# Optimization experiments

Measured on AMD Instinct MI355X. Metric: run time of the kernel, lower is better.

Reference implementation:

```python
import jax, jax.numpy as jnp
import numpy as np

BATCH = 4096
NUM_CLASSES = 10000
FEAT_DIM = 512


def setup_inputs() -> dict:
    key = jax.random.key(0)
    k1, k2, k3 = jax.random.split(key, 3)
    x = jax.random.normal(k1, (BATCH, FEAT_DIM), dtype=jnp.float32)
    labels = jax.random.randint(k2, (BATCH,), 0, NUM_CLASSES)
    centers = jax.random.normal(k3, (NUM_CLASSES, FEAT_DIM), dtype=jnp.float32)
    lr = jnp.array([0.1], dtype=jnp.float32)
    return {"x": x, "labels": labels, "centers": centers, "lr": lr}


def reference(x, labels, centers, lr):
    batch, feat_dim = x.shape
    n_classes = centers.shape[0]

    # --- center update (vectorized replacement of the per-class/per-sample double loop) ---
    # A_j = count_j * centers[j] - sum_{i: label_i==j} x_i ;  delta_j = A_j / (1 + count_j)
    ones = jnp.ones((batch,), dtype=x.dtype)
    counts = jax.ops.segment_sum(ones, labels, num_segments=n_classes)          # [C]
    sum_x = jax.ops.segment_sum(x, labels, num_segments=n_classes)              # [C, D]
    delta = (counts[:, None] * centers - sum_x) / (1.0 + counts[:, None])       # [C, D]
    # torch wraps the result in a fresh nn.Parameter -> detached from autograd graph
    centers_new = jax.lax.stop_gradient(centers - lr[0] * delta)

    # --- pairwise squared distances, then 1/(1+d) ---
    d = (jnp.sum(x * x, axis=1, keepdims=True)                                   # [B, 1]
         + jnp.sum(centers_new * centers_new, axis=1)[None, :]                   # [1, C]
         - 2.0 * (x @ centers_new.T))                                            # [B, C]
    d = 1.0 / (1.0 + d)

    # --- masked reduction: row sum minus the own-class entry, clamped ---
    row_sum = d.sum(axis=1)                                                      # [B]
    own = jnp.take_along_axis(d, labels[:, None], axis=1)[:, 0]                  # [B]
    dist = jnp.clip(row_sum - own, 1e-12, 1e12)
    return dist.mean()
```

## Files before the change

### kernel.cpp

```cpp
#include <hip/hip_runtime.h>
#include <hip/hip_bf16.h>

#define BATCH 4096
#define NCLS  10000
#define CPAD  10240
#define FDIM  512
#define MAXL  32

typedef float f32x4 __attribute__((ext_vector_type(4)));
typedef int   ix4   __attribute__((ext_vector_type(4)));
typedef int   ix8   __attribute__((ext_vector_type(8)));

__device__ static inline void gld_lds16(const void* g, void* l) {
    __builtin_amdgcn_global_load_lds(
        (const __attribute__((address_space(1))) void*)g,
        (__attribute__((address_space(3))) void*)l, 16, 0, 0);
}

__device__ static inline unsigned int fp4e(float v) {
    unsigned int s = (__float_as_uint(v) >> 31) << 3;
    float a = fabsf(v);
    unsigned int c;
    if      (a < 1.25f) c = (a < 0.75f) ? (a < 0.25f ? 0u : 1u) : 2u;
    else if (a < 2.5f)  c = (a < 1.75f) ? 3u : 4u;
    else                c = (a < 3.5f) ? 5u : (a < 5.f ? 6u : 7u);
    return s | c;
}

__device__ static inline int pdst4(int row, int k) {
    return (row >> 4) * 4096 + (k >> 7) * 1024
         + ((k >> 5) & 3) * 256 + (row & 15) * 16 + ((k & 31) >> 1);
}

__global__ void build_lists(const int* __restrict__ labels, int* __restrict__ cnt,
                            int* __restrict__ lists) {
    int i = blockIdx.x * 256 + threadIdx.x;
    int lab = labels[i];
    int p = atomicAdd(&cnt[lab], 1);
    if (p < MAXL) lists[lab * MAXL + p] = i;
}

__global__ void prep_all(const float* __restrict__ x, const int* __restrict__ cnt,
                         const int* __restrict__ lists,
                         const float* __restrict__ centers, const float* __restrict__ lr,
                         unsigned char* __restrict__ xq, float* __restrict__ xnorm,
                         unsigned char* __restrict__ cq, float* __restrict__ cnorm,
                         float* __restrict__ out) {
    const int wid = threadIdx.x >> 6, lane = threadIdx.x & 63;
    const int idx = blockIdx.x * 4 + wid;
    if (blockIdx.x == 0 && threadIdx.x == 0) out[0] = 0.f;

    if (idx < BATCH) {
        int i = idx;
        const float4* xr4 = (const float4*)&x[(size_t)i * FDIM + lane * 8];
        float4 a = xr4[0], b = xr4[1];
        unsigned int d = fp4e(a.x) | (fp4e(a.y) << 4) | (fp4e(a.z) << 8)  | (fp4e(a.w) << 12)
                       | (fp4e(b.x) << 16) | (fp4e(b.y) << 20) | (fp4e(b.z) << 24) | (fp4e(b.w) << 28);
        *(unsigned int*)(xq + pdst4(i, lane * 8)) = d;
        float s = a.x*a.x + a.y*a.y + a.z*a.z + a.w*a.w + b.x*b.x + b.y*b.y + b.z*b.z + b.w*b.w;
#pragma unroll
        for (int m = 1; m < 64; m <<= 1) s += __shfl_xor(s, m);
        if (lane == 0) xnorm[i] = s;
        return;
    }
    int j = idx - BATCH;
    if (j >= NCLS) {
        *(unsigned int*)(cq + pdst4(j, lane * 8)) = 0;
        if (lane == 0) cnorm[j] = 1e30f;
        return;
    }
    __shared__ int idxs[4][MAXL];
    int cfull = cnt[j];
    int c = cfull > MAXL ? MAXL : cfull;
    if (lane < c) idxs[wid][lane] = lists[j * MAXL + lane];
    if (lane == 0 && c > 1) {
        for (int a2 = 1; a2 < c; ++a2) {
            int v = idxs[wid][a2]; int b2 = a2 - 1;
            while (b2 >= 0 && idxs[wid][b2] > v) { idxs[wid][b2 + 1] = idxs[wid][b2]; --b2; }
            idxs[wid][b2 + 1] = v;
        }
    }
    float cf  = (float)cfull;
    float lr0 = lr[0];
    float inv = 1.f / (1.f + cf);
    const float4* cr4 = (const float4*)&centers[(size_t)j * FDIM + lane * 8];
    float4 ca = cr4[0], cb = cr4[1];
    float4 sa = {0.f, 0.f, 0.f, 0.f}, sb = {0.f, 0.f, 0.f, 0.f};
    for (int q = 0; q < c; ++q) {
        const float4* xr4 = (const float4*)&x[(size_t)idxs[wid][q] * FDIM + lane * 8];
        float4 xa = xr4[0], xb = xr4[1];
        sa.x += xa.x; sa.y += xa.y; sa.z += xa.z; sa.w += xa.w;
        sb.x += xb.x; sb.y += xb.y; sb.z += xb.z; sb.w += xb.w;
    }
    float n[8];
    n[0] = ca.x - lr0 * (cf * ca.x - sa.x) * inv;
    n[1] = ca.y - lr0 * (cf * ca.y - sa.y) * inv;
    n[2] = ca.z - lr0 * (cf * ca.z - sa.z) * inv;
    n[3] = ca.w - lr0 * (cf * ca.w - sa.w) * inv;
    n[4] = cb.x - lr0 * (cf * cb.x - sb.x) * inv;
    n[5] = cb.y - lr0 * (cf * cb.y - sb.y) * inv;
    n[6] = cb.z - lr0 * (cf * cb.z - sb.z) * inv;
    n[7] = cb.w - lr0 * (cf * cb.w - sb.w) * inv;
    unsigned int d = 0;
    float cn2 = 0.f;
#pragma unroll
    for (int q = 0; q < 8; ++q) { d |= fp4e(n[q]) << (4 * q); cn2 += n[q] * n[q]; }
    *(unsigned int*)(cq + pdst4(j, lane * 8)) = d;
#pragma unroll
    for (int m = 1; m < 64; m <<= 1) cn2 += __shfl_xor(cn2, m);
    if (lane == 0) cnorm[j] = cn2;
}

__global__ void __launch_bounds__(256, 4)
pairwise(const unsigned char* __restrict__ xq, const unsigned char* __restrict__ cq,
         const float* __restrict__ xnorm, const float* __restrict__ cnorm,
         const int* __restrict__ labels, float* __restrict__ row_part) {
    __shared__ unsigned char Als[2][8192];
    __shared__ unsigned char Bls[2][8192];
    const int tid = threadIdx.x;
    const int w = tid >> 6, lane = tid & 63;
    const int lr16 = lane & 15, lhi = lane >> 4;
    const int bid = blockIdx.x;
    const int swz = (bid & 7) * 320 + (bid >> 3);
    const int bx = swz & 31, by = swz >> 5;
    const int m_blk = bx * 128, n_blk = by * 128;
    const int mq = (w >> 1) * 64, nq = (w & 1) * 64;

    f32x4 acc[4][4];
#pragma unroll
    for (int a = 0; a < 4; ++a)
#pragma unroll
        for (int b = 0; b < 4; ++b) acc[a][b] = (f32x4)0.f;

    const unsigned char* gA[2];
    const unsigned char* gB[2];
    int ldst[2];
#pragma unroll
    for (int q = 0; q < 2; ++q) {
        gA[q] = xq + (size_t)((m_blk >> 4) + q * 4 + w) * 4096 + lane * 16;
        gB[q] = cq + (size_t)((n_blk >> 4) + q * 4 + w) * 4096 + lane * 16;
        ldst[q] = (q * 4 + w) * 1024 + lane * 16;
    }

#define STAGE(BUF, KT2) { \
    _Pragma("unroll") for (int q = 0; q < 2; ++q) { \
        gld_lds16(gA[q] + (KT2) * 1024, &Als[BUF][ldst[q]]); \
        gld_lds16(gB[q] + (KT2) * 1024, &Bls[BUF][ldst[q]]); } }

#define COMPUTE(BUF) { \
    ix8 af[4], bg[4]; \
    _Pragma("unroll") for (int mi = 0; mi < 4; ++mi) { \
        ix4 lo = *(const ix4*)&Als[BUF][((mq >> 4) + mi) * 1024 + lane * 16]; \
        af[mi] = __builtin_shufflevector(lo, lo, 0, 1, 2, 3, 0, 1, 2, 3); } \
    _Pragma("unroll") for (int ni = 0; ni < 4; ++ni) { \
        ix4 lo = *(const ix4*)&Bls[BUF][((nq >> 4) + ni) * 1024 + lane * 16]; \
        bg[ni] = __builtin_shufflevector(lo, lo, 0, 1, 2, 3, 0, 1, 2, 3); } \
    __builtin_amdgcn_s_setprio(1); \
    _Pragma("unroll") for (int mi = 0; mi < 4; ++mi) \
    _Pragma("unroll") for (int ni = 0; ni < 4; ++ni) \
        acc[mi][ni] = __builtin_amdgcn_mfma_scale_f32_16x16x128_f8f6f4( \
            bg[ni], af[mi], acc[mi][ni], 4, 4, 0, 0x7F7F7F7F, 0, 0x7F7F7F7F); \
    __builtin_amdgcn_s_setprio(0); }

    STAGE(0, 0)
#pragma unroll
    for (int t = 0; t < 3; ++t) {
        if ((t & 1) == 0) { STAGE(1, t + 1) }
        else              { STAGE(0, t + 1) }
        asm volatile("s_waitcnt vmcnt(4)" ::: "memory");
        __builtin_amdgcn_s_barrier();
        if ((t & 1) == 0) { COMPUTE(0) }
        else              { COMPUTE(1) }
        __builtin_amdgcn_sched_barrier(0);
        __builtin_amdgcn_s_barrier();
    }
    asm volatile("s_waitcnt vmcnt(0)" ::: "memory");
    __builtin_amdgcn_s_barrier();
    COMPUTE(1)

    float rsum[4];
#pragma unroll
    for (int mi = 0; mi < 4; ++mi) {
        int m_g = m_blk + mq + mi * 16 + lr16;
        float xn1 = 1.f + xnorm[m_g];
        int lab = labels[m_g];
        float s = 0.f;
#pragma unroll
        for (int ni = 0; ni < 4; ++ni) {
#pragma unroll
            for (int r = 0; r < 4; ++r) {
                int n_g = n_blk + nq + ni * 16 + lhi * 4 + r;
                float d1 = xn1 + cnorm[n_g] - 2.f * acc[mi][ni][r];
                float rc = __builtin_amdgcn_rcpf(d1);
                s += (n_g != lab) ? rc : 0.f;
            }
        }
        s += __shfl_xor(s, 16);
        s += __shfl_xor(s, 32);
        rsum[mi] = s;
    }
    __syncthreads();
    float* spart = (float*)&Als[0][0];
    if ((w & 1) && lhi == 0) {
#pragma unroll
        for (int mi = 0; mi < 4; ++mi)
            spart[mq + mi * 16 + lr16] = rsum[mi];
    }
    __syncthreads();
    if (!(w & 1) && lhi == 0) {
        float* rp = row_part + (size_t)by * BATCH + m_blk;
#pragma unroll
        for (int mi = 0; mi < 4; ++mi) {
            int ml = mq + mi * 16 + lr16;
            rp[ml] = rsum[mi] + spart[ml];
        }
    }
#undef STAGE
#undef COMPUTE
}

__global__ void finalize(const float* __restrict__ row_part, float* __restrict__ out) {
    int i = blockIdx.x * 256 + threadIdx.x;
    float s = 0.f;
    for (int p = 0; p < CPAD / 128; ++p) s += row_part[(size_t)p * BATCH + i];
    float dist = fminf(fmaxf(s, 1e-12f), 1e12f);
    float v = dist * (1.f / BATCH);
#pragma unroll
    for (int m = 1; m < 64; m <<= 1) v += __shfl_xor(v, m);
    __shared__ float red[4];
    if ((threadIdx.x & 63) == 0) red[threadIdx.x >> 6] = v;
    __syncthreads();
    if (threadIdx.x == 0) atomicAdd(out, red[0] + red[1] + red[2] + red[3]);
}

extern "C" void kernel_launch(void* const* d_in, const int* in_sizes, int n_in,
                              void* d_out, int out_size, void* d_ws, size_t ws_size,
                              hipStream_t stream) {
    const float* x       = (const float*)d_in[0];
    const int*   labels  = (const int*)d_in[1];
    const float* centers = (const float*)d_in[2];
    const float* lr      = (const float*)d_in[3];
    float* out = (float*)d_out;

    char* ws = (char*)d_ws;
    size_t off = 0;
    unsigned char* cq = (unsigned char*)(ws + off); off += (size_t)CPAD * FDIM / 2;
    unsigned char* xq = (unsigned char*)(ws + off); off += (size_t)BATCH * FDIM / 2;
    float* cnorm    = (float*)(ws + off); off += (size_t)CPAD * 4;
    float* xnorm    = (float*)(ws + off); off += (size_t)BATCH * 4;
    float* row_part = (float*)(ws + off); off += (size_t)(CPAD / 128) * BATCH * 4;
    int*   cnt      = (int*)(ws + off);   off += (size_t)NCLS * 4;
    int*   lists    = (int*)(ws + off);   off += (size_t)NCLS * MAXL * 4;

    hipMemsetAsync(cnt, 0, (size_t)NCLS * 4, stream);
    build_lists<<<BATCH / 256, 256, 0, stream>>>(labels, cnt, lists);
    prep_all<<<(BATCH + CPAD) / 4, 256, 0, stream>>>(x, cnt, lists, centers, lr,
                                                     xq, xnorm, cq, cnorm, out);
    pairwise<<<(BATCH / 128) * (CPAD / 128), 256, 0, stream>>>(xq, cq, xnorm, cnorm,
                                                               labels, row_part);
    finalize<<<BATCH / 256, 256, 0, stream>>>(row_part, out);
}
```

Before: 45.98 us.

## Shrink pairwise tile to 64x128 with all warps sharing A rows

Each pairwise block now covers 64 rows of x and 128 classes instead of a 128x128 tile. All four waves share the same 64 rows and each takes 32 columns, so the cross-wave row reduction now runs over four partials. This doubles the grid to 5120 blocks and lowers LDS and register use per block, allowing 5 blocks per CU, which should improve load balance and latency hiding. The cost is lower arithmetic intensity: the B tile is reloaded for twice as many blocks, so more global traffic per MFMA.

Result: slower. 48.83 us (+6.2%).

```diff
diff --git a/kernel.cpp b/kernel.cpp
--- a/kernel.cpp
+++ b/kernel.cpp
@@ -111,53 +111,48 @@
     if (lane == 0) cnorm[j] = cn2;
 }
 
-__global__ void __launch_bounds__(256, 4)
+__global__ void __launch_bounds__(256, 5)
 pairwise(const unsigned char* __restrict__ xq, const unsigned char* __restrict__ cq,
          const float* __restrict__ xnorm, const float* __restrict__ cnorm,
          const int* __restrict__ labels, float* __restrict__ row_part) {
-    __shared__ unsigned char Als[2][8192];
+    __shared__ unsigned char Als[2][4096];
     __shared__ unsigned char Bls[2][8192];
     const int tid = threadIdx.x;
     const int w = tid >> 6, lane = tid & 63;
     const int lr16 = lane & 15, lhi = lane >> 4;
     const int bid = blockIdx.x;
-    const int swz = (bid & 7) * 320 + (bid >> 3);
-    const int bx = swz & 31, by = swz >> 5;
-    const int m_blk = bx * 128, n_blk = by * 128;
-    const int mq = (w >> 1) * 64, nq = (w & 1) * 64;
-
-    f32x4 acc[4][4];
+    const int swz = (bid & 7) * 640 + (bid >> 3);
+    const int bx = swz & 63, by = swz >> 6;
+    const int m_blk = bx * 64, n_blk = by * 128;
+    const int nq = w * 32;
+
+    f32x4 acc[4][2];
 #pragma unroll
     for (int a = 0; a < 4; ++a)
 #pragma unroll
-        for (int b = 0; b < 4; ++b) acc[a][b] = (f32x4)0.f;
-
-    const unsigned char* gA[2];
-    const unsigned char* gB[2];
-    int ldst[2];
-#pragma unroll
-    for (int q = 0; q < 2; ++q) {
-        gA[q] = xq + (size_t)((m_blk >> 4) + q * 4 + w) * 4096 + lane * 16;
-        gB[q] = cq + (size_t)((n_blk >> 4) + q * 4 + w) * 4096 + lane * 16;
-        ldst[q] = (q * 4 + w) * 1024 + lane * 16;
-    }
+        for (int b = 0; b < 2; ++b) acc[a][b] = (f32x4)0.f;
+
+    const unsigned char* g0 = xq + (size_t)((m_blk >> 4) + (tid >> 6)) * 4096 + (tid & 63) * 16;
+    const unsigned char* g1 = cq + (size_t)((n_blk >> 4) + (tid >> 6)) * 4096 + (tid & 63) * 16;
+    const unsigned char* g2 = cq + (size_t)((n_blk >> 4) + 4 + (tid >> 6)) * 4096 + (tid & 63) * 16;
+    const int l16 = tid * 16;
 
 #define STAGE(BUF, KT2) { \
-    _Pragma("unroll") for (int q = 0; q < 2; ++q) { \
-        gld_lds16(gA[q] + (KT2) * 1024, &Als[BUF][ldst[q]]); \
-        gld_lds16(gB[q] + (KT2) * 1024, &Bls[BUF][ldst[q]]); } }
+    gld_lds16(g0 + (KT2) * 1024, &Als[BUF][l16]); \
+    gld_lds16(g1 + (KT2) * 1024, &Bls[BUF][l16]); \
+    gld_lds16(g2 + (KT2) * 1024, &Bls[BUF][4096 + l16]); }
 
 #define COMPUTE(BUF) { \
-    ix8 af[4], bg[4]; \
+    ix8 af[4], bg[2]; \
     _Pragma("unroll") for (int mi = 0; mi < 4; ++mi) { \
-        ix4 lo = *(const ix4*)&Als[BUF][((mq >> 4) + mi) * 1024 + lane * 16]; \
+        ix4 lo = *(const ix4*)&Als[BUF][mi * 1024 + lane * 16]; \
         af[mi] = __builtin_shufflevector(lo, lo, 0, 1, 2, 3, 0, 1, 2, 3); } \
-    _Pragma("unroll") for (int ni = 0; ni < 4; ++ni) { \
+    _Pragma("unroll") for (int ni = 0; ni < 2; ++ni) { \
         ix4 lo = *(const ix4*)&Bls[BUF][((nq >> 4) + ni) * 1024 + lane * 16]; \
         bg[ni] = __builtin_shufflevector(lo, lo, 0, 1, 2, 3, 0, 1, 2, 3); } \
     __builtin_amdgcn_s_setprio(1); \
     _Pragma("unroll") for (int mi = 0; mi < 4; ++mi) \
-    _Pragma("unroll") for (int ni = 0; ni < 4; ++ni) \
+    _Pragma("unroll") for (int ni = 0; ni < 2; ++ni) \
         acc[mi][ni] = __builtin_amdgcn_mfma_scale_f32_16x16x128_f8f6f4( \
             bg[ni], af[mi], acc[mi][ni], 4, 4, 0, 0x7F7F7F7F, 0, 0x7F7F7F7F); \
     __builtin_amdgcn_s_setprio(0); }
@@ -167,7 +162,7 @@
     for (int t = 0; t < 3; ++t) {
         if ((t & 1) == 0) { STAGE(1, t + 1) }
         else              { STAGE(0, t + 1) }
-        asm volatile("s_waitcnt vmcnt(4)" ::: "memory");
+        asm volatile("s_waitcnt vmcnt(3)" ::: "memory");
         __builtin_amdgcn_s_barrier();
         if ((t & 1) == 0) { COMPUTE(0) }
         else              { COMPUTE(1) }
@@ -181,12 +176,12 @@
     float rsum[4];
 #pragma unroll
     for (int mi = 0; mi < 4; ++mi) {
-        int m_g = m_blk + mq + mi * 16 + lr16;
+        int m_g = m_blk + mi * 16 + lr16;
         float xn1 = 1.f + xnorm[m_g];
         int lab = labels[m_g];
         float s = 0.f;
 #pragma unroll
-        for (int ni = 0; ni < 4; ++ni) {
+        for (int ni = 0; ni < 2; ++ni) {
 #pragma unroll
             for (int r = 0; r < 4; ++r) {
                 int n_g = n_blk + nq + ni * 16 + lhi * 4 + r;
@@ -201,18 +196,18 @@
     }
     __syncthreads();
     float* spart = (float*)&Als[0][0];
-    if ((w & 1) && lhi == 0) {
+    if (lhi == 0) {
 #pragma unroll
         for (int mi = 0; mi < 4; ++mi)
-            spart[mq + mi * 16 + lr16] = rsum[mi];
+            spart[w * 64 + mi * 16 + lr16] = rsum[mi];
     }
     __syncthreads();
-    if (!(w & 1) && lhi == 0) {
+    if (w == 0 && lhi == 0) {
         float* rp = row_part + (size_t)by * BATCH + m_blk;
 #pragma unroll
         for (int mi = 0; mi < 4; ++mi) {
-            int ml = mq + mi * 16 + lr16;
-            rp[ml] = rsum[mi] + spart[ml];
+            int ml = mi * 16 + lr16;
+            rp[ml] = spart[ml] + spart[64 + ml] + spart[128 + ml] + spart[192 + ml];
         }
     }
 #undef STAGE
@@ -256,7 +251,7 @@
     build_lists<<<BATCH / 256, 256, 0, stream>>>(labels, cnt, lists);
     prep_all<<<(BATCH + CPAD) / 4, 256, 0, stream>>>(x, cnt, lists, centers, lr,
                                                      xq, xnorm, cq, cnorm, out);
-    pairwise<<<(BATCH / 128) * (CPAD / 128), 256, 0, stream>>>(xq, cq, xnorm, cnorm,
-                                                               labels, row_part);
+    pairwise<<<(BATCH / 64) * (CPAD / 128), 256, 0, stream>>>(xq, cq, xnorm, cnorm,
+                                                              labels, row_part);
     finalize<<<BATCH / 256, 256, 0, stream>>>(row_part, out);
 }
```
